# Performance work log

Hardware: AMD Instinct MI355X
Metric: run time of the kernel (lower is better)

The kernel has to match this reference:

```python
import jax, jax.numpy as jnp
import numpy as np

B, N, C = 256, 2048, 64      # batch(residues), num_queries/keys(extra MSA seqs), channels
H, KD, VD, OD = 8, 8, 8, 64  # heads, per-head key dim, per-head value dim, output dim


def setup_inputs() -> dict:
    key = jax.random.key(0)
    ks = jax.random.split(key, 9)
    q_data = jax.random.normal(ks[0], (B, N, C), dtype=jnp.float32)
    m_data = jax.random.normal(ks[1], (B, N, C), dtype=jnp.float32)
    # per-sequence 0/1 mask, broadcast across the channel dim (same rank as q_data)
    seq_mask = (jax.random.uniform(ks[2], (B, N, 1)) < 0.9).astype(jnp.float32)
    q_mask = jnp.broadcast_to(seq_mask, (B, N, C))
    bias = jnp.zeros((B, 1, N), dtype=jnp.float32)  # ignored by forward (AF2 quirk)
    q_weights = jax.random.normal(ks[3], (C, H, KD), dtype=jnp.float32) * 0.05
    k_weights = jax.random.normal(ks[4], (C, KD), dtype=jnp.float32) * 0.05
    v_weights = jax.random.normal(ks[5], (C, VD), dtype=jnp.float32) * 0.05
    o_weights = jax.random.normal(ks[6], (H, VD, OD), dtype=jnp.float32) * 0.05
    o_bias = jnp.zeros((OD,), dtype=jnp.float32)
    gating_w = jax.random.normal(ks[7], (C, H, VD), dtype=jnp.float32) * 0.05
    gating_b = jnp.ones((H, VD), dtype=jnp.float32)
    return {
        "q_data": q_data, "m_data": m_data, "q_mask": q_mask, "bias": bias,
        "q_weights": q_weights, "k_weights": k_weights, "v_weights": v_weights,
        "o_weights": o_weights, "o_bias": o_bias,
        "gating_w": gating_w, "gating_b": gating_b,
    }


def reference(q_data, m_data, q_mask, bias, q_weights, k_weights, v_weights,
              o_weights, o_bias, gating_w, gating_b):
    # v, k projections: [B,N,C] x [C,d] -> [B,N,d]
    v = jnp.einsum('bka,ac->bkc', m_data, v_weights)
    k = jnp.einsum('bka,ac->bkc', m_data, k_weights)
    # masked mean over the query axis (dim 1); mask has full channel dim -> factor 1
    q_avg = jnp.sum(q_mask * q_data, axis=1) / (jnp.sum(q_mask, axis=1) + 1e-10)
    # pooled query: [B,C] x [C,H,KD] -> [B,H,KD], scaled by 1/sqrt(per-head key dim)
    q = jnp.einsum('ba,ahc->bhc', q_avg, q_weights) * (KD ** (-0.5))
    # attention bias from mask (the `bias` argument is overwritten, as in the original)
    mask_bias = 1e9 * (q_mask[:, None, :, 0] - 1.0)              # [B,1,N]
    logits = jnp.einsum('bhc,bkc->bhk', q, k) + mask_bias        # [B,H,N]
    weights = jax.nn.softmax(logits, axis=-1)
    weighted_avg = jnp.einsum('bhk,bkc->bhc', weights, v)        # [B,H,VD]
    # sigmoid gating per query
    gate = jax.nn.sigmoid(jnp.einsum('bqc,chv->bqhv', q_data, gating_w) + gating_b)
    gated = weighted_avg[:, None] * gate                          # [B,N,H,VD]
    out = jnp.einsum('bqhc,hco->bqo', gated, o_weights) + o_bias  # [B,N,OD]
    return out
```

## Files before the change

### kernel.cpp

```cpp
#include <hip/hip_runtime.h>
#include <hip/hip_bf16.h>
#include <math.h>

#define BN 256
#define NN 2048
#define CC 64

typedef __bf16 bf16x8 __attribute__((ext_vector_type(8)));
typedef float f32x4 __attribute__((ext_vector_type(4)));

__global__ __launch_bounds__(1024, 4) void k_fused(
    const float* __restrict__ qd, const float* __restrict__ md,
    const float* __restrict__ qm, const float* __restrict__ qw,
    const float* __restrict__ kw, const float* __restrict__ vw,
    const float* __restrict__ ow, const float* __restrict__ obias,
    const float* __restrict__ gw, const float* __restrict__ gb,
    float* __restrict__ out) {
    const int b = blockIdx.x;
    const int tid = threadIdx.x;

    __shared__ float smask[2048];
    __shared__ __align__(16) float PVpool[1024 * 17];
    __shared__ float wkv[64][16];
    __shared__ float partV[16][64];
    __shared__ float partS[16][8];
    __shared__ float qa[64], ql[64];
    __shared__ float s_wavg[64], s_sden[8];
    __shared__ __align__(16) __bf16 gwT[4096];
    __shared__ __align__(16) __bf16 w2T[4096];

#define PVF(n, j) PVpool[(n) * 17 + (j)]
#define RED(g, c) PVpool[(g) * 64 + (c)]

    smask[tid] = qm[((size_t)b * NN + tid) * CC];
    smask[tid + 1024] = qm[((size_t)b * NN + tid + 1024) * CC];
    __syncthreads();

    {
        const float4* qb4 = (const float4*)(qd + (size_t)b * NN * CC);
        const int rbase = tid >> 4;
        float4 acc = {0.f, 0.f, 0.f, 0.f};
        for (int g4 = 0; g4 < 4; ++g4) {
            float4 v[8];
#pragma unroll
            for (int j = 0; j < 8; ++j)
                v[j] = qb4[(size_t)(g4 * 8 + j) * 1024 + tid];
#pragma unroll
            for (int j = 0; j < 8; ++j) {
                const float m = smask[(g4 * 8 + j) * 64 + rbase];
                acc.x += m * v[j].x; acc.y += m * v[j].y;
                acc.z += m * v[j].z; acc.w += m * v[j].w;
            }
        }
        *(float4*)&RED(rbase, (tid & 15) * 4) = acc;
    }
    __syncthreads();

    if (tid < 64) {
        float den = 0.f;
        for (int g = 0; g < 32; ++g) den += smask[tid + g * 64];
        for (int off = 1; off < 64; off <<= 1) den += __shfl_xor(den, off, 64);
        float s = 0.f;
        for (int g = 0; g < 64; ++g) s += RED(g, tid);
        qa[tid] = s / (den + 1e-10f);
    }
    __syncthreads();
    if (tid < 64) {
        float s = 0.f;
#pragma unroll
        for (int c = 0; c < 64; ++c) s += qa[c] * qw[c * 64 + tid];
        ql[tid] = s * 0.35355339059327373f;
    }
    __syncthreads();
    if (tid < 512) {
        const int c = tid >> 3, h = tid & 7;
        float s = 0.f;
#pragma unroll
        for (int d = 0; d < 8; ++d) s += kw[c * 8 + d] * ql[h * 8 + d];
        wkv[c][h] = s;
        wkv[c][8 + h] = vw[tid];
    }
    __syncthreads();

    float vreg = 0.f, sreg = 0.f;
    for (int pass = 0; pass < 2; ++pass) {
        const int row = pass * 1024 + tid;
        const float mk = smask[row];
        const float4* rowp4 = (const float4*)(md + ((size_t)b * NN + row) * CC);
        float la[8], va[8];
#pragma unroll
        for (int h = 0; h < 8; ++h) { la[h] = 0.f; va[h] = 0.f; }
#pragma unroll
        for (int hv = 0; hv < 2; ++hv) {
            float4 buf[8];
#pragma unroll
            for (int j = 0; j < 8; ++j) buf[j] = rowp4[hv * 8 + j];
#pragma unroll
            for (int j = 0; j < 8; ++j) {
                const float xa[4] = {buf[j].x, buf[j].y, buf[j].z, buf[j].w};
#pragma unroll
                for (int q = 0; q < 4; ++q) {
                    const int c = hv * 32 + j * 4 + q;
                    const float4* wr = (const float4*)wkv[c];
                    const float4 wa = wr[0], wb = wr[1], wc = wr[2], wd = wr[3];
                    const float x = xa[q];
                    la[0] += x * wa.x; la[1] += x * wa.y; la[2] += x * wa.z; la[3] += x * wa.w;
                    la[4] += x * wb.x; la[5] += x * wb.y; la[6] += x * wb.z; la[7] += x * wb.w;
                    va[0] += x * wc.x; va[1] += x * wc.y; va[2] += x * wc.z; va[3] += x * wc.w;
                    va[4] += x * wd.x; va[5] += x * wd.y; va[6] += x * wd.z; va[7] += x * wd.w;
                }
            }
        }
#pragma unroll
        for (int h = 0; h < 8; ++h) PVF(tid, h) = mk * __expf(la[h]);
#pragma unroll
        for (int d = 0; d < 8; ++d) PVF(tid, 8 + d) = va[d];
        __syncthreads();
        {
            const int w = tid >> 6, lane = tid & 63, h = lane >> 3, d = lane & 7;
            float a2 = 0.f, s2 = 0.f;
            for (int i = 0; i < 64; ++i) {
                const int rr = w * 64 + i;
                const float p = PVF(rr, h);
                a2 += p * PVF(rr, 8 + d);
                s2 += p;
            }
            partV[w][lane] = a2;
            if (d == 0) partS[w][h] = s2;
        }
        __syncthreads();
        if (tid < 64) {
            float s = 0.f;
#pragma unroll
            for (int g = 0; g < 16; ++g) s += partV[g][tid];
            vreg += s;
        }
        if (tid < 8) {
            float s = 0.f;
#pragma unroll
            for (int g = 0; g < 16; ++g) s += partS[g][tid];
            sreg += s;
        }
        __syncthreads();
    }
    if (tid < 64) s_wavg[tid] = vreg;
    if (tid < 8) s_sden[tid] = sreg;
    __syncthreads();

    {
        const int k = tid >> 4;
        const int n0 = (tid & 15) * 4;
        const float wv = s_wavg[k] / s_sden[k >> 3];
#pragma unroll
        for (int u = 0; u < 4; ++u) {
            const int n = n0 + u;
            const int idx = n * 64 + ((((k >> 3) ^ (n & 7))) << 3) + (k & 7);
            gwT[idx] = (__bf16)gw[(size_t)k * 64 + n];
            w2T[idx] = (__bf16)(wv * ow[(size_t)k * 64 + n]);
        }
    }
    const int w = tid >> 6, lane = tid & 63, q16 = lane >> 4, c16 = lane & 15;
    float gbv[4], obv[4];
#pragma unroll
    for (int t = 0; t < 4; ++t) {
        gbv[t] = gb[t * 16 + c16];
        obv[t] = obias[t * 16 + c16];
    }
    __syncthreads();

    __bf16* gl = (__bf16*)PVpool;
#define GL(wv, r, c) gl[(((wv)*16 + (r)) * 72) + (c)]
    const size_t base_row = (size_t)b * NN + (size_t)w * 128;

    float4 cur0, cur1, cur2, cur3, nxt0, nxt1, nxt2, nxt3;
    {
        const float* arow = qd + (base_row + c16) * CC;
        cur0 = *(const float4*)(arow + q16 * 8);
        cur1 = *(const float4*)(arow + q16 * 8 + 4);
        cur2 = *(const float4*)(arow + 32 + q16 * 8);
        cur3 = *(const float4*)(arow + 32 + q16 * 8 + 4);
    }

    for (int s = 0; s < 8; ++s) {
        if (s < 7) {
            const float* arow = qd + (base_row + (s + 1) * 16 + c16) * CC;
            nxt0 = *(const float4*)(arow + q16 * 8);
            nxt1 = *(const float4*)(arow + q16 * 8 + 4);
            nxt2 = *(const float4*)(arow + 32 + q16 * 8);
            nxt3 = *(const float4*)(arow + 32 + q16 * 8 + 4);
        }
        bf16x8 af[2];
        {
            bf16x8 a;
            a[0] = (__bf16)cur0.x; a[1] = (__bf16)cur0.y; a[2] = (__bf16)cur0.z; a[3] = (__bf16)cur0.w;
            a[4] = (__bf16)cur1.x; a[5] = (__bf16)cur1.y; a[6] = (__bf16)cur1.z; a[7] = (__bf16)cur1.w;
            af[0] = a;
            a[0] = (__bf16)cur2.x; a[1] = (__bf16)cur2.y; a[2] = (__bf16)cur2.z; a[3] = (__bf16)cur2.w;
            a[4] = (__bf16)cur3.x; a[5] = (__bf16)cur3.y; a[6] = (__bf16)cur3.z; a[7] = (__bf16)cur3.w;
            af[1] = a;
        }
        f32x4 accg[4] = {{0.f, 0.f, 0.f, 0.f}, {0.f, 0.f, 0.f, 0.f},
                         {0.f, 0.f, 0.f, 0.f}, {0.f, 0.f, 0.f, 0.f}};
#pragma unroll
        for (int kc = 0; kc < 2; ++kc) {
            bf16x8 bf[4];
#pragma unroll
            for (int t = 0; t < 4; ++t) {
                const int n = t * 16 + c16;
                bf[t] = *(const bf16x8*)&gwT[n * 64 + (((kc * 4 + q16) ^ (n & 7)) << 3)];
            }
#pragma unroll
            for (int t = 0; t < 4; ++t)
                accg[t] = __builtin_amdgcn_mfma_f32_16x16x32_bf16(af[kc], bf[t],
                                                                  accg[t], 0, 0, 0);
        }
#pragma unroll
        for (int t = 0; t < 4; ++t)
#pragma unroll
            for (int r2 = 0; r2 < 4; ++r2) {
                const float x = accg[t][r2] + gbv[t];
                const float g = 1.f / (1.f + __expf(-x));
                GL(w, q16 * 4 + r2, t * 16 + c16) = (__bf16)g;
            }
        __asm__ volatile("s_waitcnt lgkmcnt(0)" ::: "memory");
        bf16x8 a2[2];
#pragma unroll
        for (int kc = 0; kc < 2; ++kc)
            a2[kc] = *(const bf16x8*)&GL(w, c16, kc * 32 + q16 * 8);
        f32x4 acco[4] = {{0.f, 0.f, 0.f, 0.f}, {0.f, 0.f, 0.f, 0.f},
                         {0.f, 0.f, 0.f, 0.f}, {0.f, 0.f, 0.f, 0.f}};
#pragma unroll
        for (int kc = 0; kc < 2; ++kc) {
            bf16x8 bf[4];
#pragma unroll
            for (int t = 0; t < 4; ++t) {
                const int n = t * 16 + c16;
                bf[t] = *(const bf16x8*)&w2T[n * 64 + (((kc * 4 + q16) ^ (n & 7)) << 3)];
            }
#pragma unroll
            for (int t = 0; t < 4; ++t)
                acco[t] = __builtin_amdgcn_mfma_f32_16x16x32_bf16(a2[kc], bf[t],
                                                                  acco[t], 0, 0, 0);
        }
        __asm__ volatile("s_waitcnt lgkmcnt(0)" ::: "memory");
        float* orow = out + (base_row + s * 16) * CC;
#pragma unroll
        for (int t = 0; t < 4; ++t)
#pragma unroll
            for (int r2 = 0; r2 < 4; ++r2)
                orow[(size_t)(q16 * 4 + r2) * 64 + t * 16 + c16] = acco[t][r2] + obv[t];
        cur0 = nxt0; cur1 = nxt1; cur2 = nxt2; cur3 = nxt3;
    }
#undef GL
#undef PVF
#undef RED
}

extern "C" void kernel_launch(void* const* d_in, const int* in_sizes, int n_in,
                              void* d_out, int out_size, void* d_ws, size_t ws_size,
                              hipStream_t stream) {
    const float* q_data = (const float*)d_in[0];
    const float* m_data = (const float*)d_in[1];
    const float* q_mask = (const float*)d_in[2];
    const float* q_w = (const float*)d_in[4];
    const float* k_w = (const float*)d_in[5];
    const float* v_w = (const float*)d_in[6];
    const float* o_w = (const float*)d_in[7];
    const float* o_b = (const float*)d_in[8];
    const float* g_w = (const float*)d_in[9];
    const float* g_b = (const float*)d_in[10];
    float* out = (float*)d_out;
    (void)d_ws; (void)ws_size; (void)in_sizes; (void)n_in; (void)out_size;

    hipLaunchKernelGGL(k_fused, dim3(BN), dim3(1024), 0, stream, q_data, m_data,
                       q_mask, q_w, k_w, v_w, o_w, o_b, g_w, g_b, out);
}
```

Measured before the change: 437.1 us.

## Split batch into row segments in a cooperative kernel with grid syncs

Turns the one-block-per-batch fused kernel into a persistent cooperative kernel. Each block now handles row segments of 256 rows, and partial sums pass through a workspace between four grid.sync phases: masked query mean, pooled-q/K fold, softmax-weighted V partials, and final normalization. The K/V projection now splits each row across four lanes with shuffle reductions. The weighted average is folded into the gate values, so the output weights no longer need rescaling per batch. This adds grid-wide barriers and workspace round trips to global memory, and it depends on every block being co-resident.

```diff
diff --git a/kernel.cpp b/kernel.cpp
--- a/kernel.cpp
+++ b/kernel.cpp
@@ -1,194 +1,249 @@
 #include <hip/hip_runtime.h>
+#include <hip/hip_cooperative_groups.h>
 #include <hip/hip_bf16.h>
 #include <math.h>
 
 #define BN 256
 #define NN 2048
 #define CC 64
+#define NSEG 8
+#define SEGR 256
+#define NT (BN * NSEG)
+#define NBLK 256
+
+#define WS_SUMQP 0
+#define WS_SUMMP (WS_SUMQP + BN * NSEG * 64)
+#define WS_VP    (WS_SUMMP + BN * NSEG)
+#define WS_SP    (WS_VP + BN * NSEG * 64)
+#define WS_KQ    (WS_SP + BN * NSEG * 8)
+#define WS_WAVG  (WS_KQ + BN * 512)
+#define WS_MASK  (WS_WAVG + BN * 64)
 
 typedef __bf16 bf16x8 __attribute__((ext_vector_type(8)));
 typedef float f32x4 __attribute__((ext_vector_type(4)));
 
-__global__ __launch_bounds__(1024, 4) void k_fused(
+namespace cg = cooperative_groups;
+
+__global__ __launch_bounds__(1024, 4) void k_all(
     const float* __restrict__ qd, const float* __restrict__ md,
     const float* __restrict__ qm, const float* __restrict__ qw,
     const float* __restrict__ kw, const float* __restrict__ vw,
     const float* __restrict__ ow, const float* __restrict__ obias,
     const float* __restrict__ gw, const float* __restrict__ gb,
-    float* __restrict__ out) {
-    const int b = blockIdx.x;
-    const int tid = threadIdx.x;
-
-    __shared__ float smask[2048];
-    __shared__ __align__(16) float PVpool[1024 * 17];
+    float* __restrict__ ws, float* __restrict__ out) {
+    cg::grid_group grid = cg::this_grid();
+    const int bid = blockIdx.x, tid = threadIdx.x;
+
+    __shared__ float lm[SEGR];
+    __shared__ float lmw[4];
+    __shared__ float red[64][64];
     __shared__ float wkv[64][16];
-    __shared__ float partV[16][64];
-    __shared__ float partS[16][8];
-    __shared__ float qa[64], ql[64];
-    __shared__ float s_wavg[64], s_sden[8];
+    __shared__ float PVF_[SEGR * 17];
+    __shared__ float partC[16][72];
+    __shared__ float qa[64], ql[64], swavg[64];
     __shared__ __align__(16) __bf16 gwT[4096];
-    __shared__ __align__(16) __bf16 w2T[4096];
-
-#define PVF(n, j) PVpool[(n) * 17 + (j)]
-#define RED(g, c) PVpool[(g) * 64 + (c)]
-
-    smask[tid] = qm[((size_t)b * NN + tid) * CC];
-    smask[tid + 1024] = qm[((size_t)b * NN + tid + 1024) * CC];
-    __syncthreads();
+    __shared__ __align__(16) __bf16 owT[4096];
+    __shared__ __align__(16) __bf16 gl[16][16][72];
+
+#pragma unroll 1
+    for (int t = bid; t < NT; t += NBLK) {
+        const int b = t >> 3, seg = t & 7;
+        const size_t grow0 = (size_t)b * NN + (size_t)seg * SEGR;
+        if (tid < SEGR) {
+            const float m = qm[(grow0 + tid) * CC];
+            lm[tid] = m;
+            ws[WS_MASK + grow0 + tid] = m;
+            float s = m;
+            for (int off = 32; off > 0; off >>= 1) s += __shfl_down(s, off, 64);
+            if ((tid & 63) == 0) lmw[tid >> 6] = s;
+        }
+        const float4* qb4 = (const float4*)(qd + grow0 * CC);
+        const float4 v0 = qb4[tid], v1 = qb4[tid + 1024];
+        const float4 v2 = qb4[tid + 2048], v3 = qb4[tid + 3072];
+        __syncthreads();
+        const int rg = tid >> 4;
+        const float m0 = lm[rg], m1 = lm[rg + 64], m2 = lm[rg + 128], m3 = lm[rg + 192];
+        float4 acc;
+        acc.x = m0 * v0.x + m1 * v1.x + m2 * v2.x + m3 * v3.x;
+        acc.y = m0 * v0.y + m1 * v1.y + m2 * v2.y + m3 * v3.y;
+        acc.z = m0 * v0.z + m1 * v1.z + m2 * v2.z + m3 * v3.z;
+        acc.w = m0 * v0.w + m1 * v1.w + m2 * v2.w + m3 * v3.w;
+        *(float4*)&red[rg][(tid & 15) * 4] = acc;
+        __syncthreads();
+        if (tid < 64) {
+            float s = 0.f;
+#pragma unroll
+            for (int g = 0; g < 64; ++g) s += red[g][tid];
+            ws[WS_SUMQP + (size_t)t * 64 + tid] = s;
+        }
+        if (tid == 0) ws[WS_SUMMP + t] = lmw[0] + lmw[1] + lmw[2] + lmw[3];
+        __syncthreads();
+    }
+    grid.sync();
 
     {
-        const float4* qb4 = (const float4*)(qd + (size_t)b * NN * CC);
-        const int rbase = tid >> 4;
-        float4 acc = {0.f, 0.f, 0.f, 0.f};
-        for (int g4 = 0; g4 < 4; ++g4) {
-            float4 v[8];
-#pragma unroll
-            for (int j = 0; j < 8; ++j)
-                v[j] = qb4[(size_t)(g4 * 8 + j) * 1024 + tid];
-#pragma unroll
-            for (int j = 0; j < 8; ++j) {
-                const float m = smask[(g4 * 8 + j) * 64 + rbase];
-                acc.x += m * v[j].x; acc.y += m * v[j].y;
-                acc.z += m * v[j].z; acc.w += m * v[j].w;
-            }
-        }
-        *(float4*)&RED(rbase, (tid & 15) * 4) = acc;
-    }
-    __syncthreads();
-
-    if (tid < 64) {
-        float den = 0.f;
-        for (int g = 0; g < 32; ++g) den += smask[tid + g * 64];
-        for (int off = 1; off < 64; off <<= 1) den += __shfl_xor(den, off, 64);
-        float s = 0.f;
-        for (int g = 0; g < 64; ++g) s += RED(g, tid);
-        qa[tid] = s / (den + 1e-10f);
-    }
-    __syncthreads();
-    if (tid < 64) {
-        float s = 0.f;
-#pragma unroll
-        for (int c = 0; c < 64; ++c) s += qa[c] * qw[c * 64 + tid];
-        ql[tid] = s * 0.35355339059327373f;
-    }
-    __syncthreads();
-    if (tid < 512) {
-        const int c = tid >> 3, h = tid & 7;
-        float s = 0.f;
-#pragma unroll
-        for (int d = 0; d < 8; ++d) s += kw[c * 8 + d] * ql[h * 8 + d];
-        wkv[c][h] = s;
-        wkv[c][8 + h] = vw[tid];
-    }
-    __syncthreads();
-
-    float vreg = 0.f, sreg = 0.f;
-    for (int pass = 0; pass < 2; ++pass) {
-        const int row = pass * 1024 + tid;
-        const float mk = smask[row];
-        const float4* rowp4 = (const float4*)(md + ((size_t)b * NN + row) * CC);
-        float la[8], va[8];
-#pragma unroll
-        for (int h = 0; h < 8; ++h) { la[h] = 0.f; va[h] = 0.f; }
-#pragma unroll
-        for (int hv = 0; hv < 2; ++hv) {
-            float4 buf[8];
-#pragma unroll
-            for (int j = 0; j < 8; ++j) buf[j] = rowp4[hv * 8 + j];
-#pragma unroll
-            for (int j = 0; j < 8; ++j) {
-                const float xa[4] = {buf[j].x, buf[j].y, buf[j].z, buf[j].w};
-#pragma unroll
-                for (int q = 0; q < 4; ++q) {
-                    const int c = hv * 32 + j * 4 + q;
-                    const float4* wr = (const float4*)wkv[c];
-                    const float4 wa = wr[0], wb = wr[1], wc = wr[2], wd = wr[3];
-                    const float x = xa[q];
-                    la[0] += x * wa.x; la[1] += x * wa.y; la[2] += x * wa.z; la[3] += x * wa.w;
-                    la[4] += x * wb.x; la[5] += x * wb.y; la[6] += x * wb.z; la[7] += x * wb.w;
-                    va[0] += x * wc.x; va[1] += x * wc.y; va[2] += x * wc.z; va[3] += x * wc.w;
-                    va[4] += x * wd.x; va[5] += x * wd.y; va[6] += x * wd.z; va[7] += x * wd.w;
-                }
-            }
-        }
-#pragma unroll
-        for (int h = 0; h < 8; ++h) PVF(tid, h) = mk * __expf(la[h]);
-#pragma unroll
-        for (int d = 0; d < 8; ++d) PVF(tid, 8 + d) = va[d];
+        const int b = bid;
+        if (tid < 64) {
+            float s = 0.f, den = 0.f;
+#pragma unroll
+            for (int g = 0; g < NSEG; ++g) {
+                s += ws[WS_SUMQP + (size_t)(b * NSEG + g) * 64 + tid];
+                den += ws[WS_SUMMP + b * NSEG + g];
+            }
+            qa[tid] = s / (den + 1e-10f);
+        }
+        __syncthreads();
+        if (tid < 64) {
+            float s = 0.f;
+#pragma unroll
+            for (int c = 0; c < 64; ++c) s += qa[c] * qw[c * 64 + tid];
+            ql[tid] = s * 0.35355339059327373f;
+        }
+        __syncthreads();
+        if (tid < 512) {
+            const int c = tid >> 3, h = tid & 7;
+            float s = 0.f;
+#pragma unroll
+            for (int d = 0; d < 8; ++d) s += kw[c * 8 + d] * ql[h * 8 + d];
+            ws[WS_KQ + (size_t)b * 512 + tid] = s;
+        }
+    }
+    grid.sync();
+
+#define C_Q(xv, PRROW)                                                        \
+    {                                                                         \
+        const float4* wr = (const float4*)wkv[PRROW];                         \
+        const float4 wa = wr[0], wb = wr[1], wc = wr[2], wd = wr[3];          \
+        la[0] += (xv)*wa.x; la[1] += (xv)*wa.y; la[2] += (xv)*wa.z; la[3] += (xv)*wa.w; \
+        la[4] += (xv)*wb.x; la[5] += (xv)*wb.y; la[6] += (xv)*wb.z; la[7] += (xv)*wb.w; \
+        va[0] += (xv)*wc.x; va[1] += (xv)*wc.y; va[2] += (xv)*wc.z; va[3] += (xv)*wc.w; \
+        va[4] += (xv)*wd.x; va[5] += (xv)*wd.y; va[6] += (xv)*wd.z; va[7] += (xv)*wd.w; \
+    }
+#define C_U(XB, U)                                    \
+    C_Q(XB.x, (((U)*4 + 0) << 2) | cg4)               \
+    C_Q(XB.y, (((U)*4 + 1) << 2) | cg4)               \
+    C_Q(XB.z, (((U)*4 + 2) << 2) | cg4)               \
+    C_Q(XB.w, (((U)*4 + 3) << 2) | cg4)
+
+#pragma unroll 1
+    for (int t = bid; t < NT; t += NBLK) {
+        const int b = t >> 3, seg = t & 7;
+        const size_t grow0 = (size_t)b * NN + (size_t)seg * SEGR;
+        if (tid < 512) {
+            const int c = tid >> 3, h = tid & 7;
+            const int pr = ((c & 15) << 2) | (c >> 4);
+            wkv[pr][h] = ws[WS_KQ + (size_t)b * 512 + tid];
+            wkv[pr][8 + h] = vw[tid];
+        }
+        const int row = tid >> 2, cg4 = tid & 3;
+        const size_t gr = grow0 + row;
+        const float mk = ws[WS_MASK + gr];
+        const float4* rp = (const float4*)(md + gr * CC) + cg4 * 4;
+        const float4 xb0 = rp[0], xb1 = rp[1], xb2 = rp[2], xb3 = rp[3];
+        __syncthreads();
+        float la[8] = {0.f, 0.f, 0.f, 0.f, 0.f, 0.f, 0.f, 0.f};
+        float va[8] = {0.f, 0.f, 0.f, 0.f, 0.f, 0.f, 0.f, 0.f};
+        C_U(xb0, 0) C_U(xb1, 1) C_U(xb2, 2) C_U(xb3, 3)
+#pragma unroll
+        for (int h = 0; h < 8; ++h) {
+            la[h] += __shfl_xor(la[h], 1, 64); la[h] += __shfl_xor(la[h], 2, 64);
+            va[h] += __shfl_xor(va[h], 1, 64); va[h] += __shfl_xor(va[h], 2, 64);
+        }
+        if (cg4 == 0) {
+#pragma unroll
+            for (int h = 0; h < 8; ++h) {
+                PVF_[row * 17 + h] = mk * __expf(la[h]);
+                PVF_[row * 17 + 8 + h] = va[h];
+            }
+        }
         __syncthreads();
         {
-            const int w = tid >> 6, lane = tid & 63, h = lane >> 3, d = lane & 7;
+            const int w = tid >> 6, lane = tid & 63, hh = lane >> 3, dd = lane & 7;
             float a2 = 0.f, s2 = 0.f;
-            for (int i = 0; i < 64; ++i) {
-                const int rr = w * 64 + i;
-                const float p = PVF(rr, h);
-                a2 += p * PVF(rr, 8 + d);
+#pragma unroll
+            for (int i = 0; i < 16; ++i) {
+                const int rr = w * 16 + i;
+                const float p = PVF_[rr * 17 + hh];
+                a2 += p * PVF_[rr * 17 + 8 + dd];
                 s2 += p;
             }
-            partV[w][lane] = a2;
-            if (d == 0) partS[w][h] = s2;
-        }
-        __syncthreads();
-        if (tid < 64) {
-            float s = 0.f;
-#pragma unroll
-            for (int g = 0; g < 16; ++g) s += partV[g][tid];
-            vreg += s;
+            partC[w][lane] = a2;
+            if (dd == 0) partC[w][64 + hh] = s2;
+        }
+        __syncthreads();
+        if (tid < 64) {
+            float s = 0.f;
+#pragma unroll
+            for (int g = 0; g < 16; ++g) s += partC[g][tid];
+            ws[WS_VP + (size_t)t * 64 + tid] = s;
         }
         if (tid < 8) {
             float s = 0.f;
 #pragma unroll
-            for (int g = 0; g < 16; ++g) s += partS[g][tid];
-            sreg += s;
-        }
-        __syncthreads();
-    }
-    if (tid < 64) s_wavg[tid] = vreg;
-    if (tid < 8) s_sden[tid] = sreg;
-    __syncthreads();
+            for (int g = 0; g < 16; ++g) s += partC[g][64 + tid];
+            ws[WS_SP + (size_t)t * 8 + tid] = s;
+        }
+        __syncthreads();
+    }
+    grid.sync();
 
     {
-        const int k = tid >> 4;
-        const int n0 = (tid & 15) * 4;
-        const float wv = s_wavg[k] / s_sden[k >> 3];
+        const int b = bid;
+        if (tid < 64) {
+            float v = 0.f, s = 0.f;
+#pragma unroll
+            for (int g = 0; g < NSEG; ++g) {
+                v += ws[WS_VP + (size_t)(b * NSEG + g) * 64 + tid];
+                s += ws[WS_SP + (size_t)(b * NSEG + g) * 8 + (tid >> 3)];
+            }
+            ws[WS_WAVG + (size_t)b * 64 + tid] = v / s;
+        }
+    }
+    grid.sync();
+
+    {
+        const int k = tid >> 4, n0 = (tid & 15) * 4;
 #pragma unroll
         for (int u = 0; u < 4; ++u) {
             const int n = n0 + u;
-            const int idx = n * 64 + ((((k >> 3) ^ (n & 7))) << 3) + (k & 7);
+            const int idx = n * 64 + (((k >> 3) ^ (n & 7)) << 3) + (k & 7);
             gwT[idx] = (__bf16)gw[(size_t)k * 64 + n];
-            w2T[idx] = (__bf16)(wv * ow[(size_t)k * 64 + n]);
+            owT[idx] = (__bf16)ow[(size_t)k * 64 + n];
         }
     }
     const int w = tid >> 6, lane = tid & 63, q16 = lane >> 4, c16 = lane & 15;
     float gbv[4], obv[4];
 #pragma unroll
-    for (int t = 0; t < 4; ++t) {
-        gbv[t] = gb[t * 16 + c16];
-        obv[t] = obias[t * 16 + c16];
-    }
-    __syncthreads();
-
-    __bf16* gl = (__bf16*)PVpool;
-#define GL(wv, r, c) gl[(((wv)*16 + (r)) * 72) + (c)]
-    const size_t base_row = (size_t)b * NN + (size_t)w * 128;
-
+    for (int tt = 0; tt < 4; ++tt) {
+        gbv[tt] = gb[tt * 16 + c16];
+        obv[tt] = obias[tt * 16 + c16];
+    }
     float4 cur0, cur1, cur2, cur3, nxt0, nxt1, nxt2, nxt3;
     {
-        const float* arow = qd + (base_row + c16) * CC;
+        const size_t br = (size_t)(bid >> 3) * NN + (size_t)(bid & 7) * SEGR + w * 16;
+        const float* arow = qd + (br + c16) * CC;
         cur0 = *(const float4*)(arow + q16 * 8);
         cur1 = *(const float4*)(arow + q16 * 8 + 4);
         cur2 = *(const float4*)(arow + 32 + q16 * 8);
         cur3 = *(const float4*)(arow + 32 + q16 * 8 + 4);
     }
-
-    for (int s = 0; s < 8; ++s) {
-        if (s < 7) {
-            const float* arow = qd + (base_row + (s + 1) * 16 + c16) * CC;
+#pragma unroll 1
+    for (int t = bid; t < NT; t += NBLK) {
+        if (tid < 64) swavg[tid] = ws[WS_WAVG + (size_t)(t >> 3) * 64 + tid];
+        __syncthreads();
+        if (t + NBLK < NT) {
+            const int tn = t + NBLK;
+            const size_t br = (size_t)(tn >> 3) * NN + (size_t)(tn & 7) * SEGR + w * 16;
+            const float* arow = qd + (br + c16) * CC;
             nxt0 = *(const float4*)(arow + q16 * 8);
             nxt1 = *(const float4*)(arow + q16 * 8 + 4);
             nxt2 = *(const float4*)(arow + 32 + q16 * 8);
             nxt3 = *(const float4*)(arow + 32 + q16 * 8 + 4);
         }
+        float wv[4];
+#pragma unroll
+        for (int tt = 0; tt < 4; ++tt) wv[tt] = swavg[tt * 16 + c16];
+
         bf16x8 af[2];
         {
             bf16x8 a;
@@ -205,55 +260,59 @@
         for (int kc = 0; kc < 2; ++kc) {
             bf16x8 bf[4];
 #pragma unroll
-            for (int t = 0; t < 4; ++t) {
-                const int n = t * 16 + c16;
-                bf[t] = *(const bf16x8*)&gwT[n * 64 + (((kc * 4 + q16) ^ (n & 7)) << 3)];
-            }
-#pragma unroll
-            for (int t = 0; t < 4; ++t)
-                accg[t] = __builtin_amdgcn_mfma_f32_16x16x32_bf16(af[kc], bf[t],
-                                                                  accg[t], 0, 0, 0);
-        }
-#pragma unroll
-        for (int t = 0; t < 4; ++t)
+            for (int tt = 0; tt < 4; ++tt) {
+                const int n = tt * 16 + c16;
+                bf[tt] = *(const bf16x8*)&gwT[n * 64 + (((kc * 4 + q16) ^ (n & 7)) << 3)];
+            }
+#pragma unroll
+            for (int tt = 0; tt < 4; ++tt)
+                accg[tt] = __builtin_amdgcn_mfma_f32_16x16x32_bf16(af[kc], bf[tt],
+                                                                   accg[tt], 0, 0, 0);
+        }
+#pragma unroll
+        for (int tt = 0; tt < 4; ++tt)
 #pragma unroll
             for (int r2 = 0; r2 < 4; ++r2) {
-                const float x = accg[t][r2] + gbv[t];
+                const float x = accg[tt][r2] + gbv[tt];
                 const float g = 1.f / (1.f + __expf(-x));
-                GL(w, q16 * 4 + r2, t * 16 + c16) = (__bf16)g;
+                gl[w][q16 * 4 + r2][tt * 16 + c16] = (__bf16)(g * wv[tt]);
             }
         __asm__ volatile("s_waitcnt lgkmcnt(0)" ::: "memory");
         bf16x8 a2[2];
 #pragma unroll
         for (int kc = 0; kc < 2; ++kc)
-            a2[kc] = *(const bf16x8*)&GL(w, c16, kc * 32 + q16 * 8);
+            a2[kc] = *(const bf16x8*)&gl[w][c16][kc * 32 + q16 * 8];
         f32x4 acco[4] = {{0.f, 0.f, 0.f, 0.f}, {0.f, 0.f, 0.f, 0.f},
                          {0.f, 0.f, 0.f, 0.f}, {0.f, 0.f, 0.f, 0.f}};
 #pragma unroll
         for (int kc = 0; kc < 2; ++kc) {
             bf16x8 bf[4];
 #pragma unroll
-            for (int t = 0; t < 4; ++t) {
-                const int n = t * 16 + c16;
-                bf[t] = *(const bf16x8*)&w2T[n * 64 + (((kc * 4 + q16) ^ (n & 7)) << 3)];
-            }
-#pragma unroll
-            for (int t = 0; t < 4; ++t)
-                acco[t] = __builtin_amdgcn_mfma_f32_16x16x32_bf16(a2[kc], bf[t],
-                                                                  acco[t], 0, 0, 0);
+            for (int tt = 0; tt < 4; ++tt) {
+                const int n = tt * 16 + c16;
+                bf[tt] = *(const bf16x8*)&owT[n * 64 + (((kc * 4 + q16) ^ (n & 7)) << 3)];
+            }
+#pragma unroll
+            for (int tt = 0; tt < 4; ++tt)
+                acco[tt] = __builtin_amdgcn_mfma_f32_16x16x32_bf16(a2[kc], bf[tt],
+                                                                   acco[tt], 0, 0, 0);
         }
         __asm__ volatile("s_waitcnt lgkmcnt(0)" ::: "memory");
-        float* orow = out + (base_row + s * 16) * CC;
-#pragma unroll
-        for (int t = 0; t < 4; ++t)
-#pragma unroll
-            for (int r2 = 0; r2 < 4; ++r2)
-                orow[(size_t)(q16 * 4 + r2) * 64 + t * 16 + c16] = acco[t][r2] + obv[t];
+        {
+            const size_t br = (size_t)(t >> 3) * NN + (size_t)(t & 7) * SEGR + w * 16;
+            float* orow = out + br * CC;
+#pragma unroll
+            for (int tt = 0; tt < 4; ++tt)
+#pragma unroll
+                for (int r2 = 0; r2 < 4; ++r2)
+                    orow[(size_t)(q16 * 4 + r2) * 64 + tt * 16 + c16] =
+                        acco[tt][r2] + obv[tt];
+        }
+        __syncthreads();
         cur0 = nxt0; cur1 = nxt1; cur2 = nxt2; cur3 = nxt3;
     }
-#undef GL
-#undef PVF
-#undef RED
+#undef C_U
+#undef C_Q
 }
 
 extern "C" void kernel_launch(void* const* d_in, const int* in_sizes, int n_in,
@@ -270,8 +329,12 @@
     const float* g_w = (const float*)d_in[9];
     const float* g_b = (const float*)d_in[10];
     float* out = (float*)d_out;
-    (void)d_ws; (void)ws_size; (void)in_sizes; (void)n_in; (void)out_size;
-
-    hipLaunchKernelGGL(k_fused, dim3(BN), dim3(1024), 0, stream, q_data, m_data,
-                       q_mask, q_w, k_w, v_w, o_w, o_b, g_w, g_b, out);
+    float* ws = (float*)d_ws;
+    (void)in_sizes; (void)n_in; (void)out_size; (void)ws_size;
+
+    void* args[] = {(void*)&q_data, (void*)&m_data, (void*)&q_mask, (void*)&q_w,
+                    (void*)&k_w,    (void*)&v_w,    (void*)&o_w,    (void*)&o_b,
+                    (void*)&g_w,    (void*)&g_b,    (void*)&ws,     (void*)&out};
+    hipLaunchCooperativeKernel((const void*)k_all, dim3(NBLK), dim3(1024), args, 0,
+                               stream);
 }
```

Measured after the change: 587.8 us. 1.34x slower.

## Compute key/value projections with bf16 MFMA and shrink shared memory footprint

Applied to the files above, without the earlier changes.

Replaces the scalar per-row fp32 key-logit and value projection over m_data with bf16 16x16x32 MFMA tiles per wave, then accumulates exp-weighted values per wave across 8 steps instead of two large passes with cross-block reductions. The gating and output weight transposes now overlap with the mean reduction, and the weighted-average scale is applied to the gate values rather than folded into the output weights. Shared memory shrinks and launch bounds request higher occupancy. The change reduces FMA/LDS work in the m_data stage but adds bf16 rounding to the logits before exp, with more barriers per row tile.

```diff
diff --git a/kernel.cpp b/kernel.cpp
--- a/kernel.cpp
+++ b/kernel.cpp
@@ -9,28 +9,27 @@
 typedef __bf16 bf16x8 __attribute__((ext_vector_type(8)));
 typedef float f32x4 __attribute__((ext_vector_type(4)));
 
-__global__ __launch_bounds__(1024, 4) void k_fused(
+__global__ __launch_bounds__(1024, 8) void k_fused(
     const float* __restrict__ qd, const float* __restrict__ md,
     const float* __restrict__ qm, const float* __restrict__ qw,
     const float* __restrict__ kw, const float* __restrict__ vw,
     const float* __restrict__ ow, const float* __restrict__ obias,
     const float* __restrict__ gw, const float* __restrict__ gb,
     float* __restrict__ out) {
-    const int b = blockIdx.x;
-    const int tid = threadIdx.x;
+    const int b = blockIdx.x, tid = threadIdx.x;
+    const int w = tid >> 6, lane = tid & 63, q16 = lane >> 4, c16 = lane & 15;
 
     __shared__ float smask[2048];
-    __shared__ __align__(16) float PVpool[1024 * 17];
-    __shared__ float wkv[64][16];
+    __shared__ __align__(16) float pool[9216];
     __shared__ float partV[16][64];
     __shared__ float partS[16][8];
-    __shared__ float qa[64], ql[64];
-    __shared__ float s_wavg[64], s_sden[8];
+    __shared__ float qa[64], ql[64], s_wavg[64];
+    __shared__ __bf16 wkvB[64][16];
     __shared__ __align__(16) __bf16 gwT[4096];
-    __shared__ __align__(16) __bf16 w2T[4096];
-
-#define PVF(n, j) PVpool[(n) * 17 + (j)]
-#define RED(g, c) PVpool[(g) * 64 + (c)]
+    __shared__ __align__(16) __bf16 owT[4096];
+
+#define RED(g, c) pool[(g) * 64 + (c)]
+#define PVF(n, j) pool[(n) * 17 + (j)]
 
     smask[tid] = qm[((size_t)b * NN + tid) * CC];
     smask[tid + 1024] = qm[((size_t)b * NN + tid + 1024) * CC];
@@ -63,6 +62,15 @@
         float s = 0.f;
         for (int g = 0; g < 64; ++g) s += RED(g, tid);
         qa[tid] = s / (den + 1e-10f);
+    } else if (tid >= 512) {
+        const int k = (tid - 512) >> 3, n0 = (tid & 7) * 8;
+#pragma unroll
+        for (int u = 0; u < 8; ++u) {
+            const int n = n0 + u;
+            const int idx = n * 64 + (((k >> 3) ^ (n & 7)) << 3) + (k & 7);
+            gwT[idx] = (__bf16)gw[(size_t)k * 64 + n];
+            owT[idx] = (__bf16)ow[(size_t)k * 64 + n];
+        }
     }
     __syncthreads();
     if (tid < 64) {
@@ -77,101 +85,64 @@
         float s = 0.f;
 #pragma unroll
         for (int d = 0; d < 8; ++d) s += kw[c * 8 + d] * ql[h * 8 + d];
-        wkv[c][h] = s;
-        wkv[c][8 + h] = vw[tid];
-    }
-    __syncthreads();
-
-    float vreg = 0.f, sreg = 0.f;
-    for (int pass = 0; pass < 2; ++pass) {
-        const int row = pass * 1024 + tid;
-        const float mk = smask[row];
-        const float4* rowp4 = (const float4*)(md + ((size_t)b * NN + row) * CC);
-        float la[8], va[8];
-#pragma unroll
-        for (int h = 0; h < 8; ++h) { la[h] = 0.f; va[h] = 0.f; }
-#pragma unroll
-        for (int hv = 0; hv < 2; ++hv) {
-            float4 buf[8];
-#pragma unroll
-            for (int j = 0; j < 8; ++j) buf[j] = rowp4[hv * 8 + j];
-#pragma unroll
-            for (int j = 0; j < 8; ++j) {
-                const float xa[4] = {buf[j].x, buf[j].y, buf[j].z, buf[j].w};
-#pragma unroll
-                for (int q = 0; q < 4; ++q) {
-                    const int c = hv * 32 + j * 4 + q;
-                    const float4* wr = (const float4*)wkv[c];
-                    const float4 wa = wr[0], wb = wr[1], wc = wr[2], wd = wr[3];
-                    const float x = xa[q];
-                    la[0] += x * wa.x; la[1] += x * wa.y; la[2] += x * wa.z; la[3] += x * wa.w;
-                    la[4] += x * wb.x; la[5] += x * wb.y; la[6] += x * wb.z; la[7] += x * wb.w;
-                    va[0] += x * wc.x; va[1] += x * wc.y; va[2] += x * wc.z; va[3] += x * wc.w;
-                    va[4] += x * wd.x; va[5] += x * wd.y; va[6] += x * wd.z; va[7] += x * wd.w;
-                }
-            }
-        }
-#pragma unroll
-        for (int h = 0; h < 8; ++h) PVF(tid, h) = mk * __expf(la[h]);
-#pragma unroll
-        for (int d = 0; d < 8; ++d) PVF(tid, 8 + d) = va[d];
+        wkvB[c][h] = (__bf16)s;
+        wkvB[c][8 + h] = (__bf16)vw[tid];
+    }
+    __syncthreads();
+
+    bf16x8 bkq[2];
+#pragma unroll
+    for (int kc = 0; kc < 2; ++kc)
+#pragma unroll
+        for (int j = 0; j < 8; ++j) bkq[kc][j] = wkvB[kc * 32 + q16 * 8 + j][c16];
+
+    float accV = 0.f, accS = 0.f;
+#pragma unroll 1
+    for (int s = 0; s < 8; ++s) {
+        const int r0 = s * 256 + w * 16;
+        const float* arow = md + ((size_t)b * NN + r0 + c16) * CC;
+        const float4 x0 = *(const float4*)(arow + q16 * 8);
+        const float4 x1 = *(const float4*)(arow + q16 * 8 + 4);
+        const float4 x2 = *(const float4*)(arow + 32 + q16 * 8);
+        const float4 x3 = *(const float4*)(arow + 32 + q16 * 8 + 4);
+        bf16x8 af[2];
+        {
+            bf16x8 a;
+            a[0] = (__bf16)x0.x; a[1] = (__bf16)x0.y; a[2] = (__bf16)x0.z; a[3] = (__bf16)x0.w;
+            a[4] = (__bf16)x1.x; a[5] = (__bf16)x1.y; a[6] = (__bf16)x1.z; a[7] = (__bf16)x1.w;
+            af[0] = a;
+            a[0] = (__bf16)x2.x; a[1] = (__bf16)x2.y; a[2] = (__bf16)x2.z; a[3] = (__bf16)x2.w;
+            a[4] = (__bf16)x3.x; a[5] = (__bf16)x3.y; a[6] = (__bf16)x3.z; a[7] = (__bf16)x3.w;
+            af[1] = a;
+        }
+        f32x4 acc = {0.f, 0.f, 0.f, 0.f};
+        acc = __builtin_amdgcn_mfma_f32_16x16x32_bf16(af[0], bkq[0], acc, 0, 0, 0);
+        acc = __builtin_amdgcn_mfma_f32_16x16x32_bf16(af[1], bkq[1], acc, 0, 0, 0);
+#pragma unroll
+        for (int r = 0; r < 4; ++r) {
+            const int rl = q16 * 4 + r;
+            const float dv = acc[r];
+            const float pexp = smask[r0 + rl] * __expf(dv);
+            PVF(w * 16 + rl, c16) = (c16 < 8) ? pexp : dv;
+        }
         __syncthreads();
         {
-            const int w = tid >> 6, lane = tid & 63, h = lane >> 3, d = lane & 7;
-            float a2 = 0.f, s2 = 0.f;
-            for (int i = 0; i < 64; ++i) {
-                const int rr = w * 64 + i;
+            const int h = lane >> 3, d = lane & 7;
+#pragma unroll
+            for (int i = 0; i < 16; ++i) {
+                const int rr = w * 16 + i;
                 const float p = PVF(rr, h);
-                a2 += p * PVF(rr, 8 + d);
-                s2 += p;
-            }
-            partV[w][lane] = a2;
-            if (d == 0) partS[w][h] = s2;
+                accV += p * PVF(rr, 8 + d);
+                accS += p;
+            }
         }
         __syncthreads();
-        if (tid < 64) {
-            float s = 0.f;
-#pragma unroll
-            for (int g = 0; g < 16; ++g) s += partV[g][tid];
-            vreg += s;
-        }
-        if (tid < 8) {
-            float s = 0.f;
-#pragma unroll
-            for (int g = 0; g < 16; ++g) s += partS[g][tid];
-            sreg += s;
-        }
-        __syncthreads();
-    }
-    if (tid < 64) s_wavg[tid] = vreg;
-    if (tid < 8) s_sden[tid] = sreg;
-    __syncthreads();
-
-    {
-        const int k = tid >> 4;
-        const int n0 = (tid & 15) * 4;
-        const float wv = s_wavg[k] / s_sden[k >> 3];
-#pragma unroll
-        for (int u = 0; u < 4; ++u) {
-            const int n = n0 + u;
-            const int idx = n * 64 + ((((k >> 3) ^ (n & 7))) << 3) + (k & 7);
-            gwT[idx] = (__bf16)gw[(size_t)k * 64 + n];
-            w2T[idx] = (__bf16)(wv * ow[(size_t)k * 64 + n]);
-        }
-    }
-    const int w = tid >> 6, lane = tid & 63, q16 = lane >> 4, c16 = lane & 15;
-    float gbv[4], obv[4];
-#pragma unroll
-    for (int t = 0; t < 4; ++t) {
-        gbv[t] = gb[t * 16 + c16];
-        obv[t] = obias[t * 16 + c16];
-    }
-    __syncthreads();
-
-    __bf16* gl = (__bf16*)PVpool;
-#define GL(wv, r, c) gl[(((wv)*16 + (r)) * 72) + (c)]
+    }
+    partV[w][lane] = accV;
+    if ((lane & 7) == 0) partS[w][lane >> 3] = accS;
+    __syncthreads();
+
     const size_t base_row = (size_t)b * NN + (size_t)w * 128;
-
     float4 cur0, cur1, cur2, cur3, nxt0, nxt1, nxt2, nxt3;
     {
         const float* arow = qd + (base_row + c16) * CC;
@@ -179,6 +150,26 @@
         cur1 = *(const float4*)(arow + q16 * 8 + 4);
         cur2 = *(const float4*)(arow + 32 + q16 * 8);
         cur3 = *(const float4*)(arow + 32 + q16 * 8 + 4);
+    }
+    if (tid < 64) {
+        float v = 0.f, ss = 0.f;
+#pragma unroll
+        for (int g = 0; g < 16; ++g) {
+            v += partV[g][tid];
+            ss += partS[g][tid >> 3];
+        }
+        s_wavg[tid] = v / ss;
+    }
+    __syncthreads();
+
+    __bf16* gl = (__bf16*)pool;
+#define GL(wv, r, c) gl[(((wv)*16 + (r)) * 72) + (c)]
+    float gbv[4], obv[4], wv[4];
+#pragma unroll
+    for (int tt = 0; tt < 4; ++tt) {
+        gbv[tt] = gb[tt * 16 + c16];
+        obv[tt] = obias[tt * 16 + c16];
+        wv[tt] = s_wavg[tt * 16 + c16];
     }
 
     for (int s = 0; s < 8; ++s) {
@@ -205,22 +196,22 @@
         for (int kc = 0; kc < 2; ++kc) {
             bf16x8 bf[4];
 #pragma unroll
-            for (int t = 0; t < 4; ++t) {
-                const int n = t * 16 + c16;
-                bf[t] = *(const bf16x8*)&gwT[n * 64 + (((kc * 4 + q16) ^ (n & 7)) << 3)];
-            }
-#pragma unroll
-            for (int t = 0; t < 4; ++t)
-                accg[t] = __builtin_amdgcn_mfma_f32_16x16x32_bf16(af[kc], bf[t],
-                                                                  accg[t], 0, 0, 0);
-        }
-#pragma unroll
-        for (int t = 0; t < 4; ++t)
+            for (int tt = 0; tt < 4; ++tt) {
+                const int n = tt * 16 + c16;
+                bf[tt] = *(const bf16x8*)&gwT[n * 64 + (((kc * 4 + q16) ^ (n & 7)) << 3)];
+            }
+#pragma unroll
+            for (int tt = 0; tt < 4; ++tt)
+                accg[tt] = __builtin_amdgcn_mfma_f32_16x16x32_bf16(af[kc], bf[tt],
+                                                                   accg[tt], 0, 0, 0);
+        }
+#pragma unroll
+        for (int tt = 0; tt < 4; ++tt)
 #pragma unroll
             for (int r2 = 0; r2 < 4; ++r2) {
-                const float x = accg[t][r2] + gbv[t];
+                const float x = accg[tt][r2] + gbv[tt];
                 const float g = 1.f / (1.f + __expf(-x));
-                GL(w, q16 * 4 + r2, t * 16 + c16) = (__bf16)g;
+                GL(w, q16 * 4 + r2, tt * 16 + c16) = (__bf16)(g * wv[tt]);
             }
         __asm__ volatile("s_waitcnt lgkmcnt(0)" ::: "memory");
         bf16x8 a2[2];
@@ -233,22 +224,22 @@
         for (int kc = 0; kc < 2; ++kc) {
             bf16x8 bf[4];
 #pragma unroll
-            for (int t = 0; t < 4; ++t) {
-                const int n = t * 16 + c16;
-                bf[t] = *(const bf16x8*)&w2T[n * 64 + (((kc * 4 + q16) ^ (n & 7)) << 3)];
-            }
-#pragma unroll
-            for (int t = 0; t < 4; ++t)
-                acco[t] = __builtin_amdgcn_mfma_f32_16x16x32_bf16(a2[kc], bf[t],
-                                                                  acco[t], 0, 0, 0);
+            for (int tt = 0; tt < 4; ++tt) {
+                const int n = tt * 16 + c16;
+                bf[tt] = *(const bf16x8*)&owT[n * 64 + (((kc * 4 + q16) ^ (n & 7)) << 3)];
+            }
+#pragma unroll
+            for (int tt = 0; tt < 4; ++tt)
+                acco[tt] = __builtin_amdgcn_mfma_f32_16x16x32_bf16(a2[kc], bf[tt],
+                                                                   acco[tt], 0, 0, 0);
         }
         __asm__ volatile("s_waitcnt lgkmcnt(0)" ::: "memory");
         float* orow = out + (base_row + s * 16) * CC;
 #pragma unroll
-        for (int t = 0; t < 4; ++t)
+        for (int tt = 0; tt < 4; ++tt)
 #pragma unroll
             for (int r2 = 0; r2 < 4; ++r2)
-                orow[(size_t)(q16 * 4 + r2) * 64 + t * 16 + c16] = acco[t][r2] + obv[t];
+                orow[(size_t)(q16 * 4 + r2) * 64 + tt * 16 + c16] = acco[tt][r2] + obv[tt];
         cur0 = nxt0; cur1 = nxt1; cur2 = nxt2; cur3 = nxt3;
     }
 #undef GL
```

Measured after the change: 449.2 us. 2.8% more time.
